# Kernel tuning notes

Hardware: AMD Instinct MI355X
Metric: run time of the kernel (lower is better)

## Reference

```python
import jax, jax.numpy as jnp
import numpy as np

ALPHA = 2.0
EPS = 1e-12  # F.normalize default eps


def setup_inputs() -> dict:
    key = jax.random.key(0)
    k1, k2 = jax.random.split(key)
    x = jax.random.normal(k1, (16, 512, 48, 48), dtype=jnp.float32)
    # 1x1 conv weight [out=1, in=C, 1, 1] flattened to [C], xavier-like scale
    w_query = jax.random.normal(k2, (512,), dtype=jnp.float32) * (2.0 / (512 + 1)) ** 0.5
    return {"x": x, "w_query": w_query}


def reference(x, w_query):
    b, c, h, w = x.shape
    n = h * w
    # attention map from detached x: 1x1 conv (dot over channels) + softplus -> [b, n]
    xd = jax.lax.stop_gradient(x)
    att = jax.nn.softplus(jnp.einsum('bchw,c->bhw', xd, w_query)).reshape(b, n)
    # L2-normalize over channel dim, flatten spatial -> [b, c, n]
    norm = jnp.sqrt(jnp.sum(x * x, axis=1, keepdims=True))
    flat = (x / jnp.maximum(norm, EPS)).reshape(b, c, n)
    # full NxN similarity, relu^alpha
    sim = jnp.einsum('bcn,bcm->bnm', flat, flat)  # [b, n, n]
    score = jnp.maximum(sim, 0.0) ** ALPHA
    # combine with attention map -> refine score per spatial location
    refine = jnp.einsum('bnm,bm->bn', score, att).reshape(b, 1, h, w)
    # weighted global average pool -> [b, c, 1, 1]
    return jnp.mean(x * refine, axis=(2, 3), keepdims=True)
```

## Files before the change

kernel.cpp:

```cpp
#include <hip/hip_runtime.h>

#define C_DIM 512
#define N_PIX 2304
#define B_DIM 16
#define K8    (C_DIM / 8)
#define K8_STRIDE (N_PIX * 8)
#define FB_STRIDE ((size_t)K8 * K8_STRIDE)

typedef float floatx4 __attribute__((ext_vector_type(4)));
typedef __bf16 bf16x8 __attribute__((ext_vector_type(8)));

static __device__ __forceinline__ unsigned short f2bf(float f) {
    unsigned u = __float_as_uint(f);
    return (unsigned short)((u + 0x7fffu + ((u >> 16) & 1u)) >> 16);
}

static __device__ __forceinline__ void load_lds16(const void* g, void* l) {
    __builtin_amdgcn_global_load_lds(
        (const __attribute__((address_space(1))) unsigned int*)g,
        (__attribute__((address_space(3))) unsigned int*)l, 16, 0, 0);
}

__global__ __launch_bounds__(256) void prep_kernel(const float* __restrict__ x,
                                                   const float* __restrict__ w,
                                                   float* __restrict__ rnorm,
                                                   float* __restrict__ normb,
                                                   float* __restrict__ att) {
    const int tid = threadIdx.x;
    const int px = tid & 63;
    const int cc = tid >> 6;
    const int pglob = blockIdx.x * 64 + px;
    const int b = pglob / N_PIX;
    const int p = pglob - b * N_PIX;

    const float* xb = x + (size_t)b * C_DIM * N_PIX + p;
    float dot = 0.f, sq = 0.f;
    #pragma unroll 4
    for (int c = cc * 128; c < cc * 128 + 128; ++c) {
        float v = xb[(size_t)c * N_PIX];
        dot = fmaf(v, w[c], dot);
        sq  = fmaf(v, v, sq);
    }
    __shared__ float sdot[4][64];
    __shared__ float ssq[4][64];
    sdot[cc][px] = dot;
    ssq[cc][px]  = sq;
    __syncthreads();
    if (cc == 0) {
        dot = sdot[0][px] + sdot[1][px] + sdot[2][px] + sdot[3][px];
        sq  = ssq[0][px]  + ssq[1][px]  + ssq[2][px]  + ssq[3][px];
        float z = dot;
        float sp = (z > 0.f) ? (z + log1pf(expf(-z))) : log1pf(expf(z));
        att[pglob] = sp;
        float nv = fmaxf(sqrtf(sq), 1e-12f);
        normb[pglob] = nv;
        rnorm[pglob] = 1.0f / nv;
    }
}

__global__ __launch_bounds__(256) void convert_kernel(const float* __restrict__ x,
                                                      const float* __restrict__ rnorm,
                                                      unsigned short* __restrict__ F) {
    const int b = blockIdx.y;
    const int t = blockIdx.x * 256 + threadIdx.x;
    const int k8 = t / 576;
    const int n4 = (t - k8 * 576) * 4;
    const float* xb = x + (size_t)b * C_DIM * N_PIX;
    const float4 rv = *(const float4*)(rnorm + b * N_PIX + n4);
    union { unsigned short u[4][8]; int4 v[4]; } cell;
    #pragma unroll
    for (int kk = 0; kk < 8; ++kk) {
        float4 xv = *(const float4*)(xb + (size_t)(k8 * 8 + kk) * N_PIX + n4);
        cell.u[0][kk] = f2bf(xv.x * rv.x);
        cell.u[1][kk] = f2bf(xv.y * rv.y);
        cell.u[2][kk] = f2bf(xv.z * rv.z);
        cell.u[3][kk] = f2bf(xv.w * rv.w);
    }
    unsigned short* dst = F + (size_t)b * FB_STRIDE + (size_t)k8 * K8_STRIDE + (size_t)n4 * 8;
    #pragma unroll
    for (int i = 0; i < 4; ++i)
        *(int4*)(dst + i * 8) = cell.v[i];
}

__global__ __launch_bounds__(256) void refine_kernel(const unsigned short* __restrict__ F,
                                                     const float* __restrict__ att,
                                                     float* __restrict__ refine) {
    const int b = blockIdx.z;
    int t = blockIdx.x, bi = 0;
    while (t >= 18 - bi) { t -= 18 - bi; ++bi; }
    const int bj = bi + t;
    const int n0 = bi * 128;
    const int m0 = bj * 128;
    const bool mirror = (bi != bj);

    const unsigned short* Fb = F + (size_t)b * FB_STRIDE;
    const float* ab = att + b * N_PIX;

    __shared__ __align__(16) unsigned short As[4 * 128 * 8];
    __shared__ __align__(16) unsigned short Bs[4 * 128 * 8];

    const int tid  = threadIdx.x;
    const int lane = tid & 63;
    const int wave = tid >> 6;
    const int wr = wave >> 1, wc = wave & 1;
    const int quad = lane >> 4, lcol = lane & 15;

    floatx4 acc[4][4];
    #pragma unroll
    for (int i = 0; i < 4; ++i)
        #pragma unroll
        for (int j = 0; j < 4; ++j)
            acc[i][j] = (floatx4)0.f;

    const unsigned short* gA = Fb + (size_t)wave * K8_STRIDE + (size_t)n0 * 8 + lane * 8;
    const unsigned short* gB = Fb + (size_t)wave * K8_STRIDE + (size_t)m0 * 8 + lane * 8;

    for (int ck = 0; ck < 16; ++ck) {
        const unsigned short* sA = gA + (size_t)ck * (4 * K8_STRIDE);
        const unsigned short* sB = gB + (size_t)ck * (4 * K8_STRIDE);
        __syncthreads();
        load_lds16(sA,       &As[wave * 1024]);
        load_lds16(sA + 512, &As[wave * 1024 + 512]);
        load_lds16(sB,       &Bs[wave * 1024]);
        load_lds16(sB + 512, &Bs[wave * 1024 + 512]);
        __syncthreads();

        bf16x8 af[4], bfr[4];
        #pragma unroll
        for (int mi = 0; mi < 4; ++mi)
            af[mi] = *(const bf16x8*)&As[(quad * 128 + wr * 64 + mi * 16 + lcol) * 8];
        #pragma unroll
        for (int ni = 0; ni < 4; ++ni)
            bfr[ni] = *(const bf16x8*)&Bs[(quad * 128 + wc * 64 + ni * 16 + lcol) * 8];
        #pragma unroll
        for (int mi = 0; mi < 4; ++mi)
            #pragma unroll
            for (int ni = 0; ni < 4; ++ni)
                acc[mi][ni] = __builtin_amdgcn_mfma_f32_16x16x32_bf16(af[mi], bfr[ni], acc[mi][ni], 0, 0, 0);
    }

    float attC[4];
    #pragma unroll
    for (int ni = 0; ni < 4; ++ni)
        attC[ni] = ab[m0 + wc * 64 + ni * 16 + lcol];

    #pragma unroll
    for (int mi = 0; mi < 4; ++mi) {
        float part[4] = {0.f, 0.f, 0.f, 0.f};
        #pragma unroll
        for (int ni = 0; ni < 4; ++ni) {
            #pragma unroll
            for (int r = 0; r < 4; ++r) {
                float s = fmaxf(acc[mi][ni][r], 0.f);
                part[r] = fmaf(s * s, attC[ni], part[r]);
            }
        }
        #pragma unroll
        for (int r = 0; r < 4; ++r) {
            float v = part[r];
            v += __shfl_xor(v, 1);
            v += __shfl_xor(v, 2);
            v += __shfl_xor(v, 4);
            v += __shfl_xor(v, 8);
            if (lcol == 0)
                atomicAdd(&refine[b * N_PIX + n0 + wr * 64 + mi * 16 + quad * 4 + r], v);
        }
    }

    if (mirror) {
        float attR[4][4];
        #pragma unroll
        for (int mi = 0; mi < 4; ++mi)
            #pragma unroll
            for (int r = 0; r < 4; ++r)
                attR[mi][r] = ab[n0 + wr * 64 + mi * 16 + quad * 4 + r];

        #pragma unroll
        for (int ni = 0; ni < 4; ++ni) {
            float msum = 0.f;
            #pragma unroll
            for (int mi = 0; mi < 4; ++mi) {
                #pragma unroll
                for (int r = 0; r < 4; ++r) {
                    float s = fmaxf(acc[mi][ni][r], 0.f);
                    msum = fmaf(s * s, attR[mi][r], msum);
                }
            }
            msum += __shfl_xor(msum, 16);
            msum += __shfl_xor(msum, 32);
            if (quad == 0)
                atomicAdd(&refine[b * N_PIX + m0 + wc * 64 + ni * 16 + lcol], msum);
        }
    }
}

__global__ __launch_bounds__(256) void refine_fallback(const float* __restrict__ x,
                                                       const float* __restrict__ rnorm,
                                                       const float* __restrict__ att,
                                                       float* __restrict__ refine) {
    const int b  = blockIdx.z;
    const int n0 = blockIdx.x * 128;
    const int m0 = blockIdx.y * 128;
    const float* xb = x + (size_t)b * C_DIM * N_PIX;
    const float* rn = rnorm + b * N_PIX;
    const float* ab = att + b * N_PIX;

    __shared__ __align__(16) unsigned short As[4 * 128 * 8];
    __shared__ __align__(16) unsigned short Bs[4 * 128 * 8];

    const int tid  = threadIdx.x;
    const int nl   = tid & 127;
    const int half = tid >> 7;
    const int lane = tid & 63;
    const int wave = tid >> 6;
    const int wr = wave >> 1, wc = wave & 1;
    const int quad = lane >> 4, lcol = lane & 15;

    const float rA = rn[n0 + nl];
    const float rB = rn[m0 + nl];

    floatx4 acc[4][4];
    #pragma unroll
    for (int i = 0; i < 4; ++i)
        #pragma unroll
        for (int j = 0; j < 4; ++j)
            acc[i][j] = (floatx4)0.f;

    for (int k0 = 0; k0 < C_DIM; k0 += 32) {
        const float* xa = xb + (size_t)(k0 + half * 16) * N_PIX;
        union { unsigned short u[16]; int4 v[2]; } ta, tb;
        #pragma unroll
        for (int j = 0; j < 16; ++j) {
            float va = xa[(size_t)j * N_PIX + n0 + nl];
            float vb = xa[(size_t)j * N_PIX + m0 + nl];
            ta.u[j] = f2bf(va * rA);
            tb.u[j] = f2bf(vb * rB);
        }
        __syncthreads();
        *(int4*)&As[((half * 2 + 0) * 128 + nl) * 8] = ta.v[0];
        *(int4*)&As[((half * 2 + 1) * 128 + nl) * 8] = ta.v[1];
        *(int4*)&Bs[((half * 2 + 0) * 128 + nl) * 8] = tb.v[0];
        *(int4*)&Bs[((half * 2 + 1) * 128 + nl) * 8] = tb.v[1];
        __syncthreads();

        bf16x8 af[4], bfr[4];
        #pragma unroll
        for (int mi = 0; mi < 4; ++mi)
            af[mi] = *(const bf16x8*)&As[(quad * 128 + wr * 64 + mi * 16 + lcol) * 8];
        #pragma unroll
        for (int ni = 0; ni < 4; ++ni)
            bfr[ni] = *(const bf16x8*)&Bs[(quad * 128 + wc * 64 + ni * 16 + lcol) * 8];
        #pragma unroll
        for (int mi = 0; mi < 4; ++mi)
            #pragma unroll
            for (int ni = 0; ni < 4; ++ni)
                acc[mi][ni] = __builtin_amdgcn_mfma_f32_16x16x32_bf16(af[mi], bfr[ni], acc[mi][ni], 0, 0, 0);
    }

    float attv[4];
    #pragma unroll
    for (int ni = 0; ni < 4; ++ni)
        attv[ni] = ab[m0 + wc * 64 + ni * 16 + lcol];

    #pragma unroll
    for (int mi = 0; mi < 4; ++mi) {
        float part[4] = {0.f, 0.f, 0.f, 0.f};
        #pragma unroll
        for (int ni = 0; ni < 4; ++ni) {
            #pragma unroll
            for (int r = 0; r < 4; ++r) {
                float s = fmaxf(acc[mi][ni][r], 0.f);
                part[r] = fmaf(s * s, attv[ni], part[r]);
            }
        }
        #pragma unroll
        for (int r = 0; r < 4; ++r) {
            float v = part[r];
            v += __shfl_xor(v, 1);
            v += __shfl_xor(v, 2);
            v += __shfl_xor(v, 4);
            v += __shfl_xor(v, 8);
            if (lcol == 0)
                atomicAdd(&refine[b * N_PIX + n0 + wr * 64 + mi * 16 + quad * 4 + r], v);
        }
    }
}

__global__ __launch_bounds__(256) void pool_kernel(const unsigned short* __restrict__ F,
                                                   const float* __restrict__ refine,
                                                   const float* __restrict__ normb,
                                                   float* __restrict__ out) {
    const int lane = threadIdx.x & 63;
    const int wave = threadIdx.x >> 6;
    const int g = blockIdx.x * 4 + wave;
    const int b = g >> 6;
    const int k8 = g & 63;
    const unsigned short* Fr = F + (size_t)b * FB_STRIDE + (size_t)k8 * K8_STRIDE;
    const float* rf = refine + b * N_PIX;
    const float* nb = normb + b * N_PIX;
    float s[8] = {0.f, 0.f, 0.f, 0.f, 0.f, 0.f, 0.f, 0.f};
    #pragma unroll 4
    for (int j = 0; j < 36; ++j) {
        const int n = j * 64 + lane;
        bf16x8 fv = *(const bf16x8*)(Fr + (size_t)n * 8);
        float rr = rf[n] * nb[n];
        #pragma unroll
        for (int kk = 0; kk < 8; ++kk)
            s[kk] = fmaf((float)fv[kk], rr, s[kk]);
    }
    #pragma unroll
    for (int kk = 0; kk < 8; ++kk) {
        float v = s[kk];
        #pragma unroll
        for (int off = 32; off > 0; off >>= 1) v += __shfl_down(v, off);
        if (lane == 0) out[b * C_DIM + k8 * 8 + kk] = v * (1.0f / N_PIX);
    }
}

__global__ __launch_bounds__(256) void pool_fallback(const float* __restrict__ x,
                                                     const float* __restrict__ refine,
                                                     float* __restrict__ out) {
    const int lane = threadIdx.x & 63;
    const int wave = threadIdx.x >> 6;
    const int g = blockIdx.x * 4 + wave;
    const int b = g >> 9;
    const float4* xr = (const float4*)(x + (size_t)g * N_PIX);
    const float4* rr = (const float4*)(refine + (size_t)b * N_PIX);
    float s = 0.f;
    #pragma unroll
    for (int j = 0; j < 9; ++j) {
        float4 xv = xr[j * 64 + lane];
        float4 rv = rr[j * 64 + lane];
        s += xv.x * rv.x + xv.y * rv.y + xv.z * rv.z + xv.w * rv.w;
    }
    #pragma unroll
    for (int off = 32; off > 0; off >>= 1) s += __shfl_down(s, off);
    if (lane == 0) out[g] = s * (1.0f / N_PIX);
}

extern "C" void kernel_launch(void* const* d_in, const int* in_sizes, int n_in,
                              void* d_out, int out_size, void* d_ws, size_t ws_size,
                              hipStream_t stream) {
    const float* x = (const float*)d_in[0];
    const float* w = (const float*)d_in[1];
    float* rnorm  = (float*)d_ws;
    float* normb  = rnorm + B_DIM * N_PIX;
    float* att    = normb + B_DIM * N_PIX;
    float* refine = att + B_DIM * N_PIX;
    unsigned short* F = (unsigned short*)(refine + B_DIM * N_PIX);
    float* out    = (float*)d_out;

    const size_t need = (size_t)4 * B_DIM * N_PIX * 4 + (size_t)B_DIM * FB_STRIDE * 2;

    hipMemsetAsync(refine, 0, B_DIM * N_PIX * sizeof(float), stream);
    prep_kernel<<<dim3(B_DIM * N_PIX / 64), 256, 0, stream>>>(x, w, rnorm, normb, att);
    if (ws_size >= need) {
        convert_kernel<<<dim3(144, B_DIM), 256, 0, stream>>>(x, rnorm, F);
        refine_kernel<<<dim3(171, 1, B_DIM), 256, 0, stream>>>(F, att, refine);
        pool_kernel<<<dim3(B_DIM * K8 / 4), 256, 0, stream>>>(F, refine, normb, out);
    } else {
        refine_fallback<<<dim3(18, 18, B_DIM), 256, 0, stream>>>(x, rnorm, att, refine);
        pool_fallback<<<dim3(B_DIM * C_DIM / 4), 256, 0, stream>>>(x, refine, out);
    }
}
```

Measured before the change: 212.2 us.

## Fuse prep and bf16 conversion, remap refine blocks per XCD, deepen K tile

Merges the norm/attention prep kernel with the bf16 packing kernel, so each block converts its 64 pixels right after computing their inverse norms. This removes one launch and a second pass over x, much of which should then hit cache. The refine kernel now uses a flat grid mapped so each batch's tiles land on one XCD for L2 locality. It also loads 8 K-blocks per sync instead of 4, halving barrier count at the cost of twice the LDS. The fused kernel's conversion stage has lower parallelism per block.

Result: no change. 210.8 us (-0.7%).

```diff
diff --git a/kernel.cpp b/kernel.cpp
--- a/kernel.cpp
+++ b/kernel.cpp
@@ -21,28 +21,31 @@
         (__attribute__((address_space(3))) unsigned int*)l, 16, 0, 0);
 }
 
-__global__ __launch_bounds__(256) void prep_kernel(const float* __restrict__ x,
-                                                   const float* __restrict__ w,
-                                                   float* __restrict__ rnorm,
-                                                   float* __restrict__ normb,
-                                                   float* __restrict__ att) {
+__global__ __launch_bounds__(256) void prep_convert_kernel(const float* __restrict__ x,
+                                                           const float* __restrict__ w,
+                                                           float* __restrict__ rnorm,
+                                                           float* __restrict__ normb,
+                                                           float* __restrict__ att,
+                                                           unsigned short* __restrict__ F) {
     const int tid = threadIdx.x;
     const int px = tid & 63;
     const int cc = tid >> 6;
-    const int pglob = blockIdx.x * 64 + px;
-    const int b = pglob / N_PIX;
-    const int p = pglob - b * N_PIX;
-
-    const float* xb = x + (size_t)b * C_DIM * N_PIX + p;
+    const int b  = (blockIdx.x * 64) / N_PIX;
+    const int p0 = (blockIdx.x * 64) % N_PIX;
+    const int p  = p0 + px;
+
+    const float* xb = x + (size_t)b * C_DIM * N_PIX;
+
     float dot = 0.f, sq = 0.f;
     #pragma unroll 4
     for (int c = cc * 128; c < cc * 128 + 128; ++c) {
-        float v = xb[(size_t)c * N_PIX];
+        float v = xb[(size_t)c * N_PIX + p];
         dot = fmaf(v, w[c], dot);
         sq  = fmaf(v, v, sq);
     }
     __shared__ float sdot[4][64];
     __shared__ float ssq[4][64];
+    __shared__ __align__(16) float srn[64];
     sdot[cc][px] = dot;
     ssq[cc][px]  = sq;
     __syncthreads();
@@ -51,42 +54,47 @@
         sq  = ssq[0][px]  + ssq[1][px]  + ssq[2][px]  + ssq[3][px];
         float z = dot;
         float sp = (z > 0.f) ? (z + log1pf(expf(-z))) : log1pf(expf(z));
-        att[pglob] = sp;
+        att[b * N_PIX + p] = sp;
         float nv = fmaxf(sqrtf(sq), 1e-12f);
-        normb[pglob] = nv;
-        rnorm[pglob] = 1.0f / nv;
-    }
-}
-
-__global__ __launch_bounds__(256) void convert_kernel(const float* __restrict__ x,
-                                                      const float* __restrict__ rnorm,
-                                                      unsigned short* __restrict__ F) {
-    const int b = blockIdx.y;
-    const int t = blockIdx.x * 256 + threadIdx.x;
-    const int k8 = t / 576;
-    const int n4 = (t - k8 * 576) * 4;
-    const float* xb = x + (size_t)b * C_DIM * N_PIX;
-    const float4 rv = *(const float4*)(rnorm + b * N_PIX + n4);
-    union { unsigned short u[4][8]; int4 v[4]; } cell;
-    #pragma unroll
-    for (int kk = 0; kk < 8; ++kk) {
-        float4 xv = *(const float4*)(xb + (size_t)(k8 * 8 + kk) * N_PIX + n4);
-        cell.u[0][kk] = f2bf(xv.x * rv.x);
-        cell.u[1][kk] = f2bf(xv.y * rv.y);
-        cell.u[2][kk] = f2bf(xv.z * rv.z);
-        cell.u[3][kk] = f2bf(xv.w * rv.w);
-    }
-    unsigned short* dst = F + (size_t)b * FB_STRIDE + (size_t)k8 * K8_STRIDE + (size_t)n4 * 8;
-    #pragma unroll
-    for (int i = 0; i < 4; ++i)
-        *(int4*)(dst + i * 8) = cell.v[i];
+        normb[b * N_PIX + p] = nv;
+        float rv = 1.0f / nv;
+        rnorm[b * N_PIX + p] = rv;
+        srn[px] = rv;
+    }
+    __syncthreads();
+
+    const int n4l = tid & 15;
+    const int k8b = tid >> 4;
+    const float4 rv4 = *(const float4*)&srn[n4l * 4];
+    #pragma unroll
+    for (int it = 0; it < 4; ++it) {
+        const int k8 = k8b + 16 * it;
+        union { unsigned short u[4][8]; int4 v[4]; } cell;
+        #pragma unroll
+        for (int kk = 0; kk < 8; ++kk) {
+            float4 xv = *(const float4*)(xb + (size_t)(k8 * 8 + kk) * N_PIX + p0 + n4l * 4);
+            cell.u[0][kk] = f2bf(xv.x * rv4.x);
+            cell.u[1][kk] = f2bf(xv.y * rv4.y);
+            cell.u[2][kk] = f2bf(xv.z * rv4.z);
+            cell.u[3][kk] = f2bf(xv.w * rv4.w);
+        }
+        unsigned short* dst = F + (size_t)b * FB_STRIDE + (size_t)k8 * K8_STRIDE
+                            + (size_t)(p0 + n4l * 4) * 8;
+        #pragma unroll
+        for (int i = 0; i < 4; ++i)
+            *(int4*)(dst + i * 8) = cell.v[i];
+    }
 }
 
 __global__ __launch_bounds__(256) void refine_kernel(const unsigned short* __restrict__ F,
                                                      const float* __restrict__ att,
                                                      float* __restrict__ refine) {
-    const int b = blockIdx.z;
-    int t = blockIdx.x, bi = 0;
+    const int id   = blockIdx.x;
+    const int xcd  = id & 7;
+    const int slot = id >> 3;
+    const int hi   = (slot >= 171) ? 1 : 0;
+    const int b    = xcd + 8 * hi;
+    int t = slot - 171 * hi, bi = 0;
     while (t >= 18 - bi) { t -= 18 - bi; ++bi; }
     const int bj = bi + t;
     const int n0 = bi * 128;
@@ -96,8 +104,8 @@
     const unsigned short* Fb = F + (size_t)b * FB_STRIDE;
     const float* ab = att + b * N_PIX;
 
-    __shared__ __align__(16) unsigned short As[4 * 128 * 8];
-    __shared__ __align__(16) unsigned short Bs[4 * 128 * 8];
+    __shared__ __align__(16) unsigned short As[8 * 128 * 8];
+    __shared__ __align__(16) unsigned short Bs[8 * 128 * 8];
 
     const int tid  = threadIdx.x;
     const int lane = tid & 63;
@@ -112,31 +120,38 @@
         for (int j = 0; j < 4; ++j)
             acc[i][j] = (floatx4)0.f;
 
-    const unsigned short* gA = Fb + (size_t)wave * K8_STRIDE + (size_t)n0 * 8 + lane * 8;
-    const unsigned short* gB = Fb + (size_t)wave * K8_STRIDE + (size_t)m0 * 8 + lane * 8;
-
-    for (int ck = 0; ck < 16; ++ck) {
-        const unsigned short* sA = gA + (size_t)ck * (4 * K8_STRIDE);
-        const unsigned short* sB = gB + (size_t)ck * (4 * K8_STRIDE);
+    for (int ck = 0; ck < 8; ++ck) {
         __syncthreads();
-        load_lds16(sA,       &As[wave * 1024]);
-        load_lds16(sA + 512, &As[wave * 1024 + 512]);
-        load_lds16(sB,       &Bs[wave * 1024]);
-        load_lds16(sB + 512, &Bs[wave * 1024 + 512]);
+        #pragma unroll
+        for (int h = 0; h < 2; ++h) {
+            const int kbl = wave * 2 + h;
+            const unsigned short* sA = Fb + (size_t)(ck * 8 + kbl) * K8_STRIDE
+                                     + (size_t)n0 * 8 + lane * 8;
+            const unsigned short* sB = Fb + (size_t)(ck * 8 + kbl) * K8_STRIDE
+                                     + (size_t)m0 * 8 + lane * 8;
+            load_lds16(sA,       &As[kbl * 1024]);
+            load_lds16(sA + 512, &As[kbl * 1024 + 512]);
+            load_lds16(sB,       &Bs[kbl * 1024]);
+            load_lds16(sB + 512, &Bs[kbl * 1024 + 512]);
+        }
         __syncthreads();
 
-        bf16x8 af[4], bfr[4];
-        #pragma unroll
-        for (int mi = 0; mi < 4; ++mi)
-            af[mi] = *(const bf16x8*)&As[(quad * 128 + wr * 64 + mi * 16 + lcol) * 8];
-        #pragma unroll
-        for (int ni = 0; ni < 4; ++ni)
-            bfr[ni] = *(const bf16x8*)&Bs[(quad * 128 + wc * 64 + ni * 16 + lcol) * 8];
-        #pragma unroll
-        for (int mi = 0; mi < 4; ++mi)
+        #pragma unroll
+        for (int h = 0; h < 2; ++h) {
+            const int kb = h * 4 + quad;
+            bf16x8 af[4], bfr[4];
+            #pragma unroll
+            for (int mi = 0; mi < 4; ++mi)
+                af[mi] = *(const bf16x8*)&As[(kb * 128 + wr * 64 + mi * 16 + lcol) * 8];
             #pragma unroll
             for (int ni = 0; ni < 4; ++ni)
-                acc[mi][ni] = __builtin_amdgcn_mfma_f32_16x16x32_bf16(af[mi], bfr[ni], acc[mi][ni], 0, 0, 0);
+                bfr[ni] = *(const bf16x8*)&Bs[(kb * 128 + wc * 64 + ni * 16 + lcol) * 8];
+            #pragma unroll
+            for (int mi = 0; mi < 4; ++mi)
+                #pragma unroll
+                for (int ni = 0; ni < 4; ++ni)
+                    acc[mi][ni] = __builtin_amdgcn_mfma_f32_16x16x32_bf16(af[mi], bfr[ni], acc[mi][ni], 0, 0, 0);
+        }
     }
 
     float attC[4];
@@ -338,6 +353,43 @@
     if (lane == 0) out[g] = s * (1.0f / N_PIX);
 }
 
+__global__ __launch_bounds__(256) void prep_kernel(const float* __restrict__ x,
+                                                   const float* __restrict__ w,
+                                                   float* __restrict__ rnorm,
+                                                   float* __restrict__ normb,
+                                                   float* __restrict__ att) {
+    const int tid = threadIdx.x;
+    const int px = tid & 63;
+    const int cc = tid >> 6;
+    const int pglob = blockIdx.x * 64 + px;
+    const int b = pglob / N_PIX;
+    const int p = pglob - b * N_PIX;
+
+    const float* xb = x + (size_t)b * C_DIM * N_PIX + p;
+    float dot = 0.f, sq = 0.f;
+    #pragma unroll 4
+    for (int c = cc * 128; c < cc * 128 + 128; ++c) {
+        float v = xb[(size_t)c * N_PIX];
+        dot = fmaf(v, w[c], dot);
+        sq  = fmaf(v, v, sq);
+    }
+    __shared__ float sdot[4][64];
+    __shared__ float ssq[4][64];
+    sdot[cc][px] = dot;
+    ssq[cc][px]  = sq;
+    __syncthreads();
+    if (cc == 0) {
+        dot = sdot[0][px] + sdot[1][px] + sdot[2][px] + sdot[3][px];
+        sq  = ssq[0][px]  + ssq[1][px]  + ssq[2][px]  + ssq[3][px];
+        float z = dot;
+        float sp = (z > 0.f) ? (z + log1pf(expf(-z))) : log1pf(expf(z));
+        att[pglob] = sp;
+        float nv = fmaxf(sqrtf(sq), 1e-12f);
+        normb[pglob] = nv;
+        rnorm[pglob] = 1.0f / nv;
+    }
+}
+
 extern "C" void kernel_launch(void* const* d_in, const int* in_sizes, int n_in,
                               void* d_out, int out_size, void* d_ws, size_t ws_size,
                               hipStream_t stream) {
@@ -353,12 +405,12 @@
     const size_t need = (size_t)4 * B_DIM * N_PIX * 4 + (size_t)B_DIM * FB_STRIDE * 2;
 
     hipMemsetAsync(refine, 0, B_DIM * N_PIX * sizeof(float), stream);
-    prep_kernel<<<dim3(B_DIM * N_PIX / 64), 256, 0, stream>>>(x, w, rnorm, normb, att);
     if (ws_size >= need) {
-        convert_kernel<<<dim3(144, B_DIM), 256, 0, stream>>>(x, rnorm, F);
-        refine_kernel<<<dim3(171, 1, B_DIM), 256, 0, stream>>>(F, att, refine);
+        prep_convert_kernel<<<dim3(B_DIM * N_PIX / 64), 256, 0, stream>>>(x, w, rnorm, normb, att, F);
+        refine_kernel<<<dim3(171 * 16), 256, 0, stream>>>(F, att, refine);
         pool_kernel<<<dim3(B_DIM * K8 / 4), 256, 0, stream>>>(F, refine, normb, out);
     } else {
+        prep_kernel<<<dim3(B_DIM * N_PIX / 64), 256, 0, stream>>>(x, w, rnorm, normb, att);
         refine_fallback<<<dim3(18, 18, B_DIM), 256, 0, stream>>>(x, rnorm, att, refine);
         pool_fallback<<<dim3(B_DIM * C_DIM / 4), 256, 0, stream>>>(x, refine, out);
     }
```
